# Kernel optimization log

Hardware: AMD Instinct MI355X
Metric: run time of the kernel (lower is better)

Reference implementation:

```python
import jax, jax.numpy as jnp
import numpy as np

BASIS_PRIMES = (2, 3, 5, 7, 11, 13, 17, 19, 23, 29)


def _build_resonance(max_seq):
    # p-adic valuations v_p(n) for n = 1..max_seq, each basis prime (vectorized LUT build)
    n = np.arange(1, max_seq + 1, dtype=np.int64)
    vals = np.zeros((max_seq, len(BASIS_PRIMES)), dtype=np.float32)
    for j, p in enumerate(BASIS_PRIMES):
        m = n.copy()
        while True:
            div = (m % p) == 0
            if not div.any():
                break
            vals[div, j] += 1.0
            m = np.where(div, m // p, m)
    # resonance(a,b) = sum_i min(v_{p_i}(a), v_{p_i}(b))  -> [T, T]
    res = np.zeros((max_seq, max_seq), dtype=np.float32)
    for j in range(len(BASIS_PRIMES)):
        vj = vals[:, j]
        res += np.minimum(vj[:, None], vj[None, :])
    causal = np.tril(np.ones((max_seq, max_seq), dtype=bool))
    allowed = ((res > 0) | np.eye(max_seq, dtype=bool)) & causal
    bias = (np.log1p(res) * allowed).astype(np.float32)
    return bias, allowed


def setup_inputs() -> dict:
    B, T, d_model, head_size, max_seq = 8, 2048, 1024, 128, 2048
    key = jax.random.key(0)
    kx, kq, kk, kv = jax.random.split(key, 4)
    bound = 1.0 / np.sqrt(d_model)  # torch Linear default init range
    x = jax.random.normal(kx, (B, T, d_model), dtype=jnp.float32)
    Wq = jax.random.uniform(kq, (head_size, d_model), jnp.float32, -bound, bound)
    Wk = jax.random.uniform(kk, (head_size, d_model), jnp.float32, -bound, bound)
    Wv = jax.random.uniform(kv, (head_size, d_model), jnp.float32, -bound, bound)
    bias, allowed = _build_resonance(max_seq)
    return {
        "x": x, "Wq": Wq, "Wk": Wk, "Wv": Wv,
        "resonance_bias": jnp.asarray(bias),
        "allowed": jnp.asarray(allowed),
    }


def reference(x, Wq, Wk, Wv, resonance_bias, allowed):
    B, T, C = x.shape
    q = jnp.einsum('btc,hc->bth', x, Wq)
    k = jnp.einsum('btc,hc->bth', x, Wk)
    v = jnp.einsum('btc,hc->bth', x, Wv)
    # NOTE: original scales by C**-0.5 where C = d_model (input channels)
    wei = jnp.einsum('bth,bsh->bts', q, k) * (C ** -0.5)
    wei = wei + resonance_bias[:T, :T]
    neg = jnp.finfo(wei.dtype).min
    wei = jnp.where(allowed[:T, :T], wei, neg)
    wei = jax.nn.softmax(wei, axis=-1)  # dropout is identity in eval mode
    return jnp.einsum('bts,bsh->bth', wei, v)
```

## Files before the change

kernel.cpp:

```cpp
#include <hip/hip_runtime.h>
#include <hip/hip_bf16.h>
#include <stdint.h>

typedef float f32x4  __attribute__((ext_vector_type(4)));
typedef short s16x8  __attribute__((ext_vector_type(8)));
typedef short s16x4  __attribute__((ext_vector_type(4)));
typedef unsigned short u16x8 __attribute__((ext_vector_type(8)));

#define MFMA16(A,B,C) __builtin_amdgcn_mfma_f32_16x16x32_bf16((A),(B),(C),0,0,0)

__device__ __forceinline__ short f2bf(float f) {
    uint32_t u = __float_as_uint(f);
    u += 0x7FFFu + ((u >> 16) & 1u);
    return (short)(u >> 16);
}
__device__ __forceinline__ float bf2f(unsigned short u) {
    return __uint_as_float(((uint32_t)u) << 16);
}
__device__ __forceinline__ uint32_t cvtpk(float a, float b) {
  uint32_t r;
  asm("v_cvt_pk_bf16_f32 %0, %1, %2" : "=v"(r) : "v"(a), "v"(b));
  return r;
}
__device__ __forceinline__ int cum_jobs(int qt) {
  int h = qt >> 1;
  return (qt & 1) ? (h + 1) * (h + 1) : h * (h + 1);
}

#define OFF_PB   0u
#define OFF_WPK  8388608u
#define OFF_PQ   9175040u
#define OFF_PK   13369344u
#define OFF_PV   17563648u
#define OFF_PML  21757952u
#define OFF_PO   22863872u
#define WS_SPLIT 60096512u

__global__ __launch_bounds__(256) void pack_misc_kernel(
    const float* __restrict__ wq, const float* __restrict__ wk,
    const float* __restrict__ wv, const float* __restrict__ bias,
    short* __restrict__ Wpk, short* __restrict__ pb) {
  const int tid = threadIdx.x, wid = tid >> 6, lane = tid & 63;
  const int g = lane >> 4, c4 = lane & 15;
  if (blockIdx.x < 192) {
    const int idx = blockIdx.x * 4 + wid;
    const int im = idx >> 8, rest = idx & 255;
    const int ntl = rest >> 5, k32 = rest & 31;
    const float* w = (im == 0) ? wq : (im == 1) ? wk : wv;
    const float* p = w + (size_t)(ntl * 16 + c4) * 1024 + k32 * 32 + 4 * g;
    f32x4 lo = *(const f32x4*)p;
    f32x4 hi = *(const f32x4*)(p + 16);
    s16x8 o = { f2bf(lo[0]), f2bf(lo[1]), f2bf(lo[2]), f2bf(lo[3]),
                f2bf(hi[0]), f2bf(hi[1]), f2bf(hi[2]), f2bf(hi[3]) };
    *(s16x8*)(Wpk + (size_t)idx * 512 + lane * 8) = o;
  } else {
    const int idx = (blockIdx.x - 192) * 4 + wid;
    const int t16 = idx >> 6, s32 = idx & 63;
    const int t = t16 * 16 + c4;
    const int sb = s32 * 32 + 4 * g;
    const float* p = bias + (size_t)t * 2048 + sb;
    f32x4 lo = *(const f32x4*)p;
    f32x4 hi = *(const f32x4*)(p + 16);
    s16x8 o;
    #pragma unroll
    for (int i = 0; i < 4; ++i) {
      int s0 = sb + i, s1 = sb + 16 + i;
      bool ok0 = (s0 <= t) && (s0 == t || lo[i] > 0.f);
      bool ok1 = (s1 <= t) && (s1 == t || hi[i] > 0.f);
      o[i]     = f2bf(ok0 ? lo[i] : -1e30f);
      o[4 + i] = f2bf(ok1 ? hi[i] : -1e30f);
    }
    *(s16x8*)(pb + (size_t)idx * 512 + lane * 8) = o;
  }
}

__global__ __launch_bounds__(256, 2) void qkv_gemm12_kernel(
    const float* __restrict__ x, const short* __restrict__ Wpk,
    short* __restrict__ pq, short* __restrict__ pk, short* __restrict__ pv) {
  __shared__ short lx[2][12288];
  const int tid = threadIdx.x, wid = tid >> 6, lane = tid & 63;
  const int g = lane >> 4, c4 = lane & 15;
  const int L8 = lane * 8;
  const int x8 = blockIdx.x & 7, q = blockIdx.x >> 3;
  const int im = q % 3, rt = (q / 3) * 8 + x8;
  const int b = rt >> 4;
  const int h = wid & 1, ch = wid >> 1;

#define G12_STAGE(buf, kk) { \
    _Pragma("unroll") \
    for (int i = 0; i < 6; ++i) { \
      const int u = wid * 6 + i; \
      if (u < 16) { \
        const int a = u >> 1, hf = u & 1; \
        const float* src = x + (size_t)(rt * 128 + a * 16 + c4) * 1024 \
                         + (size_t)(kk) * 32 + 4 * g + hf * 16; \
        __builtin_amdgcn_global_load_lds( \
            (const __attribute__((address_space(1))) void*)src, \
            (__attribute__((address_space(3))) void*)&lx[buf][(2*a+hf)*512], \
            16, 0, 0); \
      } else { \
        const int n = u - 16; \
        const short* src = Wpk + (size_t)(im * 256 + n * 32 + (kk)) * 512 + L8; \
        __builtin_amdgcn_global_load_lds( \
            (const __attribute__((address_space(1))) void*)src, \
            (__attribute__((address_space(3))) void*)&lx[buf][8192 + n * 512], \
            16, 0, 0); \
      } \
    } }

  f32x4 acc[4][4];
  #pragma unroll
  for (int tt = 0; tt < 4; ++tt)
    #pragma unroll
    for (int nn = 0; nn < 4; ++nn) acc[tt][nn] = (f32x4){0.f, 0.f, 0.f, 0.f};

  G12_STAGE(0, 0)
  __syncthreads();

  union CV { uint32_t u[4]; s16x8 v; };

#define G12_BODY(SWAPPED)                                                    \
  for (int k = 0; k < 32; ++k) {                                             \
    const int cur = k & 1;                                                   \
    if (k < 31) G12_STAGE(cur ^ 1, k + 1)                                    \
    s16x8 af[4], bfr[4];                                                     \
    _Pragma("unroll")                                                        \
    for (int tt = 0; tt < 4; ++tt) {                                         \
      const int a = h * 4 + tt;                                              \
      f32x4 alo = *(const f32x4*)&lx[cur][(2 * a) * 512 + L8];               \
      f32x4 ahi = *(const f32x4*)&lx[cur][(2 * a + 1) * 512 + L8];           \
      CV t;                                                                  \
      t.u[0] = cvtpk(alo[0], alo[1]); t.u[1] = cvtpk(alo[2], alo[3]);        \
      t.u[2] = cvtpk(ahi[0], ahi[1]); t.u[3] = cvtpk(ahi[2], ahi[3]);        \
      af[tt] = t.v;                                                          \
    }                                                                        \
    _Pragma("unroll")                                                        \
    for (int nn = 0; nn < 4; ++nn)                                           \
      bfr[nn] = *(const s16x8*)&lx[cur][8192 + (ch * 4 + nn) * 512 + L8];    \
    _Pragma("unroll")                                                        \
    for (int tt = 0; tt < 4; ++tt)                                           \
      _Pragma("unroll")                                                      \
      for (int nn = 0; nn < 4; ++nn)                                         \
        acc[tt][nn] = SWAPPED ? MFMA16(bfr[nn], af[tt], acc[tt][nn])         \
                              : MFMA16(af[tt], bfr[nn], acc[tt][nn]);        \
    __syncthreads();                                                         \
  }

  if (im < 2) {
    G12_BODY(1)
    short* __restrict__ o = (im == 1) ? pk : pq;
    #pragma unroll
    for (int tt = 0; tt < 4; ++tt) {
      const int q16 = (rt & 15) * 8 + h * 4 + tt;
      #pragma unroll
      for (int fl = 0; fl < 2; ++fl) {
        const int f = ch * 2 + fl;
        s16x8 fr = { f2bf(acc[tt][2*fl][0]),   f2bf(acc[tt][2*fl][1]),
                     f2bf(acc[tt][2*fl][2]),   f2bf(acc[tt][2*fl][3]),
                     f2bf(acc[tt][2*fl+1][0]), f2bf(acc[tt][2*fl+1][1]),
                     f2bf(acc[tt][2*fl+1][2]), f2bf(acc[tt][2*fl+1][3]) };
        *(s16x8*)(o + (size_t)(b * 512 + q16 * 4 + f) * 512 + L8) = fr;
      }
    }
  } else {
    G12_BODY(0)
    #pragma unroll
    for (int pr = 0; pr < 2; ++pr) {
      const int s32 = (rt & 15) * 4 + h * 2 + pr;
      #pragma unroll
      for (int nn = 0; nn < 4; ++nn) {
        const int nt = ch * 4 + nn;
        s16x8 fr = { f2bf(acc[2*pr][nn][0]),   f2bf(acc[2*pr][nn][1]),
                     f2bf(acc[2*pr][nn][2]),   f2bf(acc[2*pr][nn][3]),
                     f2bf(acc[2*pr+1][nn][0]), f2bf(acc[2*pr+1][nn][1]),
                     f2bf(acc[2*pr+1][nn][2]), f2bf(acc[2*pr+1][nn][3]) };
        *(s16x8*)(pv + (size_t)(b * 512 + s32 * 8 + nt) * 512 + L8) = fr;
      }
    }
  }
#undef G12_BODY
#undef G12_STAGE
}

template<bool SPLIT>
__global__ __launch_bounds__(128) void attn_kernel(
    const short* __restrict__ pq, const short* __restrict__ pk,
    const short* __restrict__ pv, const short* __restrict__ pb,
    float* __restrict__ out, float* __restrict__ part_ml,
    short* __restrict__ part_o) {
  int qt, c;
  if (SPLIT) {
    const int i = blockIdx.x;
    int h = (int)sqrtf((float)i);
    while (h * h > i) --h;
    while ((h + 1) * (h + 1) <= i) ++h;
    if (i < h * (h + 1)) { qt = 2 * h - 1; c = i - h * h; }
    else                 { qt = 2 * h;     c = i - h * (h + 1); }
  } else {
    qt = blockIdx.x; c = 0;
  }
  const int n = (qt >> 1) + 1;
  const int tid = threadIdx.x;
  const int wid = tid >> 6, lane = tid & 63;
  const int g = lane >> 4, c4 = lane & 15;
  const int b = blockIdx.y;
  const int q16a = qt * 4 + wid * 2;
  const int L8 = lane * 8;

  s16x8 qfa[4], qfb[4];
  #pragma unroll
  for (int f = 0; f < 4; ++f) {
    qfa[f] = *(const s16x8*)(pq + (size_t)(b * 512 + q16a * 4 + f) * 512 + L8);
    qfb[f] = *(const s16x8*)(pq + (size_t)(b * 512 + (q16a + 1) * 4 + f) * 512 + L8);
  }

  float m0 = -1e30f, l0 = 0.f, m1 = -1e30f, l1 = 0.f;
  f32x4 acc0[8], acc1[8];
  #pragma unroll
  for (int i = 0; i < 8; ++i) {
    acc0[i] = (f32x4){0.f, 0.f, 0.f, 0.f};
    acc1[i] = (f32x4){0.f, 0.f, 0.f, 0.f};
  }

  const int q_hi_w = qt * 64 + wid * 32 + 32;
  const int s_begin = SPLIT ? c * 128 : 0;
  const int s_stop  = min(SPLIT ? s_begin + 128 : (1 << 30), q_hi_w);

  for (int s0 = s_begin; s0 < s_stop; s0 += 32) {
    const int s16i = s0 >> 4, s32 = s0 >> 5;
    const short* kbase = pk + (size_t)(b * 512 + s16i * 4) * 512 + L8;
    const short* vbase = pv + (size_t)(b * 512 + s32 * 8) * 512 + L8;
    s16x8 kf0[4], kf1[4];
    #pragma unroll
    for (int f = 0; f < 4; ++f) {
      kf0[f] = *(const s16x8*)(kbase + (size_t)f * 512);
      kf1[f] = *(const s16x8*)(kbase + (size_t)(4 + f) * 512);
    }
    u16x8 bva = *(const u16x8*)(pb + (size_t)(q16a * 64 + s32) * 512 + L8);
    u16x8 bvb = *(const u16x8*)(pb + (size_t)((q16a + 1) * 64 + s32) * 512 + L8);
    f32x4 s0a = (f32x4){0.f,0.f,0.f,0.f}, s1a = (f32x4){0.f,0.f,0.f,0.f};
    f32x4 s0b = (f32x4){0.f,0.f,0.f,0.f}, s1b = (f32x4){0.f,0.f,0.f,0.f};
    __builtin_amdgcn_s_setprio(1);
    #pragma unroll
    for (int f = 0; f < 4; ++f) {
      s0a = MFMA16(kf0[f], qfa[f], s0a);
      s1a = MFMA16(kf1[f], qfa[f], s1a);
      s0b = MFMA16(kf0[f], qfb[f], s0b);
      s1b = MFMA16(kf1[f], qfb[f], s1b);
    }
    __builtin_amdgcn_s_setprio(0);
    float va[8], vb[8];
    #pragma unroll
    for (int st = 0; st < 2; ++st)
      #pragma unroll
      for (int r = 0; r < 4; ++r) {
        va[st * 4 + r] = (st ? s1a[r] : s0a[r]) * 0.03125f + bf2f(bva[st * 4 + r]);
        vb[st * 4 + r] = (st ? s1b[r] : s0b[r]) * 0.03125f + bf2f(bvb[st * 4 + r]);
      }
    float mva = va[0], mvb = vb[0];
    #pragma unroll
    for (int i = 1; i < 8; ++i) { mva = fmaxf(mva, va[i]); mvb = fmaxf(mvb, vb[i]); }
    mva = fmaxf(mva, __shfl_xor(mva, 16)); mva = fmaxf(mva, __shfl_xor(mva, 32));
    mvb = fmaxf(mvb, __shfl_xor(mvb, 16)); mvb = fmaxf(mvb, __shfl_xor(mvb, 32));
    if (!__all((mva <= m0 + 8.f) && (mvb <= m1 + 8.f))) {
      float mn0 = fmaxf(m0, mva), mn1 = fmaxf(m1, mvb);
      float a0 = __expf(m0 - mn0), a1 = __expf(m1 - mn1);
      l0 *= a0; l1 *= a1; m0 = mn0; m1 = mn1;
      float ar0[4], ar1[4];
      #pragma unroll
      for (int r = 0; r < 4; ++r) {
        ar0[r] = __shfl(a0, (lane & 48) | (4 * g + r));
        ar1[r] = __shfl(a1, (lane & 48) | (4 * g + r));
      }
      #pragma unroll
      for (int nt = 0; nt < 8; ++nt)
        #pragma unroll
        for (int r = 0; r < 4; ++r) {
          acc0[nt][r] *= ar0[r];
          acc1[nt][r] *= ar1[r];
        }
    }
    float pa8[8], pb8[8], psa = 0.f, psb = 0.f;
    #pragma unroll
    for (int i = 0; i < 8; ++i) {
      pa8[i] = (va[i] > -1e29f) ? __expf(va[i] - m0) : 0.f;  psa += pa8[i];
      pb8[i] = (vb[i] > -1e29f) ? __expf(vb[i] - m1) : 0.f;  psb += pb8[i];
    }
    psa += __shfl_xor(psa, 16); psa += __shfl_xor(psa, 32); l0 += psa;
    psb += __shfl_xor(psb, 16); psb += __shfl_xor(psb, 32); l1 += psb;
    s16x8 paf = { f2bf(pa8[0]), f2bf(pa8[1]), f2bf(pa8[2]), f2bf(pa8[3]),
                  f2bf(pa8[4]), f2bf(pa8[5]), f2bf(pa8[6]), f2bf(pa8[7]) };
    s16x8 pbf = { f2bf(pb8[0]), f2bf(pb8[1]), f2bf(pb8[2]), f2bf(pb8[3]),
                  f2bf(pb8[4]), f2bf(pb8[5]), f2bf(pb8[6]), f2bf(pb8[7]) };
    __builtin_amdgcn_s_setprio(1);
    #pragma unroll
    for (int nt = 0; nt < 8; ++nt) {
      s16x8 vf = *(const s16x8*)(vbase + (size_t)nt * 512);
      acc0[nt] = MFMA16(paf, vf, acc0[nt]);
      acc1[nt] = MFMA16(pbf, vf, acc1[nt]);
    }
    __builtin_amdgcn_s_setprio(0);
  }

  if (!SPLIT || n == 1) {
    float li0 = 1.f / l0, li1 = 1.f / l1;
    float lr0[4], lr1[4];
    #pragma unroll
    for (int r = 0; r < 4; ++r) {
      lr0[r] = __shfl(li0, (lane & 48) | (4 * g + r));
      lr1[r] = __shfl(li1, (lane & 48) | (4 * g + r));
    }
    const int row0 = qt * 64 + wid * 32;
    #pragma unroll
    for (int nt = 0; nt < 8; ++nt)
      #pragma unroll
      for (int r = 0; r < 4; ++r) {
        out[(size_t)(b * 2048 + row0 + 4 * g + r) * 128 + 16 * nt + c4] =
            acc0[nt][r] * lr0[r];
        out[(size_t)(b * 2048 + row0 + 16 + 4 * g + r) * 128 + 16 * nt + c4] =
            acc1[nt][r] * lr1[r];
      }
  } else {
    const int slot = b * 270 + cum_jobs(qt) - 2 + c;
    short* po = part_o + (size_t)slot * 8192 + (size_t)(wid * 8) * 512 + L8;
    #pragma unroll
    for (int nt = 0; nt < 8; ++nt) {
      s16x8 fr = { f2bf(acc0[nt][0]), f2bf(acc0[nt][1]),
                   f2bf(acc0[nt][2]), f2bf(acc0[nt][3]),
                   f2bf(acc1[nt][0]), f2bf(acc1[nt][1]),
                   f2bf(acc1[nt][2]), f2bf(acc1[nt][3]) };
      *(s16x8*)(po + (size_t)nt * 512) = fr;
    }
    if (lane < 16) {
      part_ml[slot * 128 + wid * 32 + c4]           = m0;
      part_ml[slot * 128 + wid * 32 + 16 + c4]      = m1;
      part_ml[slot * 128 + 64 + wid * 32 + c4]      = l0;
      part_ml[slot * 128 + 64 + wid * 32 + 16 + c4] = l1;
    }
  }
}

__global__ __launch_bounds__(256) void combine_kernel(
    const float* __restrict__ part_ml, const unsigned short* __restrict__ part_o,
    float* __restrict__ out) {
  const int qt = 2 + blockIdx.x;
  const int b = blockIdx.y;
  const int n = (qt >> 1) + 1;
  const int slot0 = b * 270 + cum_jobs(qt) - 2;
  const int tid = threadIdx.x;

  __shared__ float scl[16][64];
  if (tid < 64) {
    const int r = tid;
    float M = -1e30f;
    for (int cc = 0; cc < n; ++cc)
      M = fmaxf(M, part_ml[(size_t)(slot0 + cc) * 128 + r]);
    float L = 0.f;
    for (int cc = 0; cc < n; ++cc)
      L += part_ml[(size_t)(slot0 + cc) * 128 + 64 + r] *
           __expf(part_ml[(size_t)(slot0 + cc) * 128 + r] - M);
    float inv = 1.f / L;
    for (int cc = 0; cc < n; ++cc)
      scl[cc][r] = __expf(part_ml[(size_t)(slot0 + cc) * 128 + r] - M) * inv;
  }
  __syncthreads();
  const int fgr = tid >> 6, lane = tid & 63;
  const int g = lane >> 4, c4 = lane & 15;
  for (int ff = fgr; ff < 16; ff += 4) {
    const int rbase = (ff >> 3) * 32 + 4 * g;
    const int col = (ff & 7) * 16 + c4;
    float o[8] = {0.f,0.f,0.f,0.f,0.f,0.f,0.f,0.f};
    for (int cc = 0; cc < n; ++cc) {
      u16x8 v = *(const u16x8*)(part_o +
          (size_t)(slot0 + cc) * 8192 + (size_t)ff * 512 + lane * 8);
      #pragma unroll
      for (int j = 0; j < 8; ++j)
        o[j] += bf2f(v[j]) * scl[cc][rbase + (j >> 2) * 16 + (j & 3)];
    }
    #pragma unroll
    for (int j = 0; j < 8; ++j) {
      const int row = rbase + (j >> 2) * 16 + (j & 3);
      out[(size_t)(b * 2048 + qt * 64 + row) * 128 + col] = o[j];
    }
  }
}

extern "C" void kernel_launch(void* const* d_in, const int* in_sizes, int n_in,
                              void* d_out, int out_size, void* d_ws, size_t ws_size,
                              hipStream_t stream) {
  const float* x    = (const float*)d_in[0];
  const float* wq   = (const float*)d_in[1];
  const float* wk   = (const float*)d_in[2];
  const float* wv   = (const float*)d_in[3];
  const float* bias = (const float*)d_in[4];

  char* ws = (char*)d_ws;
  short* pb      = (short*)(ws + OFF_PB);
  short* Wpk     = (short*)(ws + OFF_WPK);
  short* pq      = (short*)(ws + OFF_PQ);
  short* pk      = (short*)(ws + OFF_PK);
  short* pv      = (short*)(ws + OFF_PV);
  float* part_ml = (float*)(ws + OFF_PML);
  short* part_o  = (short*)(ws + OFF_PO);
  float* outp    = (float*)d_out;

  pack_misc_kernel<<<2240, 256, 0, stream>>>(wq, wk, wv, bias, Wpk, pb);
  qkv_gemm12_kernel<<<384, 256, 0, stream>>>(x, Wpk, pq, pk, pv);

  if (ws_size >= WS_SPLIT) {
    attn_kernel<true><<<dim3(272, 8), 128, 0, stream>>>(
        pq, pk, pv, pb, outp, part_ml, part_o);
    combine_kernel<<<dim3(30, 8), 256, 0, stream>>>(
        part_ml, (const unsigned short*)part_o, outp);
  } else {
    attn_kernel<false><<<dim3(32, 8), 128, 0, stream>>>(
        pq, pk, pv, pb, outp, part_ml, part_o);
  }
}
```

Measured before the change: 97.19 us.

## Pre-pack x to bf16 in pack kernel and shrink QKV GEMM tile

Converts x from fp32 to bf16 MFMA-fragment layout inside the packing kernel, written into workspace that overlaps the later attention partial buffers. The QKV GEMM then loads packed bf16 x directly, with no in-loop conversion. It also moves to 128-thread blocks with a 64-row tile and twice as many blocks. This removes the per-k conversion work and halves the bytes of x each GEMM block reads. The cost is an extra full pass over x and more re-reads of the weight tiles.

Measured after the change: 97.70 us. About the same (+0.5%).

```diff
diff --git a/kernel.cpp b/kernel.cpp
--- a/kernel.cpp
+++ b/kernel.cpp
@@ -16,11 +16,6 @@
 }
 __device__ __forceinline__ float bf2f(unsigned short u) {
     return __uint_as_float(((uint32_t)u) << 16);
-}
-__device__ __forceinline__ uint32_t cvtpk(float a, float b) {
-  uint32_t r;
-  asm("v_cvt_pk_bf16_f32 %0, %1, %2" : "=v"(r) : "v"(a), "v"(b));
-  return r;
 }
 __device__ __forceinline__ int cum_jobs(int qt) {
   int h = qt >> 1;
@@ -32,14 +27,16 @@
 #define OFF_PQ   9175040u
 #define OFF_PK   13369344u
 #define OFF_PV   17563648u
+#define OFF_XPK  21757952u
 #define OFF_PML  21757952u
 #define OFF_PO   22863872u
 #define WS_SPLIT 60096512u
 
-__global__ __launch_bounds__(256) void pack_misc_kernel(
+__global__ __launch_bounds__(256) void pack_all_kernel(
     const float* __restrict__ wq, const float* __restrict__ wk,
     const float* __restrict__ wv, const float* __restrict__ bias,
-    short* __restrict__ Wpk, short* __restrict__ pb) {
+    const float* __restrict__ x, short* __restrict__ Wpk,
+    short* __restrict__ pb, short* __restrict__ xpk) {
   const int tid = threadIdx.x, wid = tid >> 6, lane = tid & 63;
   const int g = lane >> 4, c4 = lane & 15;
   if (blockIdx.x < 192) {
@@ -53,7 +50,7 @@
     s16x8 o = { f2bf(lo[0]), f2bf(lo[1]), f2bf(lo[2]), f2bf(lo[3]),
                 f2bf(hi[0]), f2bf(hi[1]), f2bf(hi[2]), f2bf(hi[3]) };
     *(s16x8*)(Wpk + (size_t)idx * 512 + lane * 8) = o;
-  } else {
+  } else if (blockIdx.x < 2240) {
     const int idx = (blockIdx.x - 192) * 4 + wid;
     const int t16 = idx >> 6, s32 = idx & 63;
     const int t = t16 * 16 + c4;
@@ -71,39 +68,46 @@
       o[4 + i] = f2bf(ok1 ? hi[i] : -1e30f);
     }
     *(s16x8*)(pb + (size_t)idx * 512 + lane * 8) = o;
-  }
-}
-
-__global__ __launch_bounds__(256, 2) void qkv_gemm12_kernel(
-    const float* __restrict__ x, const short* __restrict__ Wpk,
+  } else {
+    const int idx = (blockIdx.x - 2240) * 4 + wid;
+    const int m16 = idx >> 5, k32 = idx & 31;
+    const float* p = x + (size_t)(m16 * 16 + c4) * 1024 + k32 * 32 + 4 * g;
+    f32x4 lo = *(const f32x4*)p;
+    f32x4 hi = *(const f32x4*)(p + 16);
+    s16x8 o = { f2bf(lo[0]), f2bf(lo[1]), f2bf(lo[2]), f2bf(lo[3]),
+                f2bf(hi[0]), f2bf(hi[1]), f2bf(hi[2]), f2bf(hi[3]) };
+    *(s16x8*)(xpk + (size_t)idx * 512 + lane * 8) = o;
+  }
+}
+
+__global__ __launch_bounds__(128, 2) void qkv_gemm13_kernel(
+    const short* __restrict__ xpk, const short* __restrict__ Wpk,
     short* __restrict__ pq, short* __restrict__ pk, short* __restrict__ pv) {
-  __shared__ short lx[2][12288];
+  __shared__ short lx[2][6144];
   const int tid = threadIdx.x, wid = tid >> 6, lane = tid & 63;
   const int g = lane >> 4, c4 = lane & 15;
   const int L8 = lane * 8;
   const int x8 = blockIdx.x & 7, q = blockIdx.x >> 3;
   const int im = q % 3, rt = (q / 3) * 8 + x8;
-  const int b = rt >> 4;
-  const int h = wid & 1, ch = wid >> 1;
-
-#define G12_STAGE(buf, kk) { \
+  const int b = rt >> 5;
+  const int ch = wid;
+
+#define G13_STAGE(buf, kk) { \
     _Pragma("unroll") \
     for (int i = 0; i < 6; ++i) { \
       const int u = wid * 6 + i; \
-      if (u < 16) { \
-        const int a = u >> 1, hf = u & 1; \
-        const float* src = x + (size_t)(rt * 128 + a * 16 + c4) * 1024 \
-                         + (size_t)(kk) * 32 + 4 * g + hf * 16; \
+      if (u < 4) { \
+        const short* src = xpk + (size_t)((rt * 4 + u) * 32 + (kk)) * 512 + L8; \
         __builtin_amdgcn_global_load_lds( \
             (const __attribute__((address_space(1))) void*)src, \
-            (__attribute__((address_space(3))) void*)&lx[buf][(2*a+hf)*512], \
+            (__attribute__((address_space(3))) void*)&lx[buf][u * 512], \
             16, 0, 0); \
       } else { \
-        const int n = u - 16; \
+        const int n = u - 4; \
         const short* src = Wpk + (size_t)(im * 256 + n * 32 + (kk)) * 512 + L8; \
         __builtin_amdgcn_global_load_lds( \
             (const __attribute__((address_space(1))) void*)src, \
-            (__attribute__((address_space(3))) void*)&lx[buf][8192 + n * 512], \
+            (__attribute__((address_space(3))) void*)&lx[buf][2048 + n * 512], \
             16, 0, 0); \
       } \
     } }
@@ -114,29 +118,20 @@
     #pragma unroll
     for (int nn = 0; nn < 4; ++nn) acc[tt][nn] = (f32x4){0.f, 0.f, 0.f, 0.f};
 
-  G12_STAGE(0, 0)
+  G13_STAGE(0, 0)
   __syncthreads();
 
-  union CV { uint32_t u[4]; s16x8 v; };
-
-#define G12_BODY(SWAPPED)                                                    \
+#define G13_BODY(SWAPPED)                                                    \
   for (int k = 0; k < 32; ++k) {                                             \
     const int cur = k & 1;                                                   \
-    if (k < 31) G12_STAGE(cur ^ 1, k + 1)                                    \
+    if (k < 31) G13_STAGE(cur ^ 1, k + 1)                                    \
     s16x8 af[4], bfr[4];                                                     \
     _Pragma("unroll")                                                        \
-    for (int tt = 0; tt < 4; ++tt) {                                         \
-      const int a = h * 4 + tt;                                              \
-      f32x4 alo = *(const f32x4*)&lx[cur][(2 * a) * 512 + L8];               \
-      f32x4 ahi = *(const f32x4*)&lx[cur][(2 * a + 1) * 512 + L8];           \
-      CV t;                                                                  \
-      t.u[0] = cvtpk(alo[0], alo[1]); t.u[1] = cvtpk(alo[2], alo[3]);        \
-      t.u[2] = cvtpk(ahi[0], ahi[1]); t.u[3] = cvtpk(ahi[2], ahi[3]);        \
-      af[tt] = t.v;                                                          \
-    }                                                                        \
+    for (int tt = 0; tt < 4; ++tt)                                           \
+      af[tt] = *(const s16x8*)&lx[cur][tt * 512 + L8];                       \
     _Pragma("unroll")                                                        \
     for (int nn = 0; nn < 4; ++nn)                                           \
-      bfr[nn] = *(const s16x8*)&lx[cur][8192 + (ch * 4 + nn) * 512 + L8];    \
+      bfr[nn] = *(const s16x8*)&lx[cur][2048 + (ch * 4 + nn) * 512 + L8];    \
     _Pragma("unroll")                                                        \
     for (int tt = 0; tt < 4; ++tt)                                           \
       _Pragma("unroll")                                                      \
@@ -147,11 +142,11 @@
   }
 
   if (im < 2) {
-    G12_BODY(1)
+    G13_BODY(1)
     short* __restrict__ o = (im == 1) ? pk : pq;
     #pragma unroll
     for (int tt = 0; tt < 4; ++tt) {
-      const int q16 = (rt & 15) * 8 + h * 4 + tt;
+      const int q16 = (rt & 31) * 4 + tt;
       #pragma unroll
       for (int fl = 0; fl < 2; ++fl) {
         const int f = ch * 2 + fl;
@@ -163,10 +158,10 @@
       }
     }
   } else {
-    G12_BODY(0)
+    G13_BODY(0)
     #pragma unroll
     for (int pr = 0; pr < 2; ++pr) {
-      const int s32 = (rt & 15) * 4 + h * 2 + pr;
+      const int s32 = (rt & 31) * 2 + pr;
       #pragma unroll
       for (int nn = 0; nn < 4; ++nn) {
         const int nt = ch * 4 + nn;
@@ -178,8 +173,8 @@
       }
     }
   }
-#undef G12_BODY
-#undef G12_STAGE
+#undef G13_BODY
+#undef G13_STAGE
 }
 
 template<bool SPLIT>
@@ -400,12 +395,13 @@
   short* pq      = (short*)(ws + OFF_PQ);
   short* pk      = (short*)(ws + OFF_PK);
   short* pv      = (short*)(ws + OFF_PV);
+  short* xpk     = (short*)(ws + OFF_XPK);
   float* part_ml = (float*)(ws + OFF_PML);
   short* part_o  = (short*)(ws + OFF_PO);
   float* outp    = (float*)d_out;
 
-  pack_misc_kernel<<<2240, 256, 0, stream>>>(wq, wk, wv, bias, Wpk, pb);
-  qkv_gemm12_kernel<<<384, 256, 0, stream>>>(x, Wpk, pq, pk, pv);
+  pack_all_kernel<<<10432, 256, 0, stream>>>(wq, wk, wv, bias, x, Wpk, pb, xpk);
+  qkv_gemm13_kernel<<<768, 128, 0, stream>>>(xpk, Wpk, pq, pk, pv);
 
   if (ws_size >= WS_SPLIT) {
     attn_kernel<true><<<dim3(272, 8), 128, 0, stream>>>(
```
